# Kernel tuning notes

Hardware: AMD Instinct MI355X
Metric: run time of the kernel (lower is better)

## Reference

```python
import jax, jax.numpy as jnp
import numpy as np

NUM_CAPS_OUT = 10
NUM_NODES = 32 * 6 * 6  # 1152
IN_DIM = 8
OUT_DIM = 16
ROUTING_ITERS = 3


def squash(x):
    # scale = |x|^2/(1+|x|^2); out = scale * x/|x|  (no epsilon, faithful to torch)
    sn = jnp.sum(x * x, axis=-1, keepdims=True)
    return sn / (1.0 + sn) * x / jnp.sqrt(sn)


def setup_inputs() -> dict:
    key = jax.random.key(0)
    ks = jax.random.split(key, 6)
    B = 512
    images = jax.random.normal(ks[0], (B, 1, 28, 28), dtype=jnp.float32)
    # ConvLayer: Conv2d(1, 256, k=9, s=1) with bias
    conv1_w = jax.random.normal(ks[1], (256, 1, 9, 9), dtype=jnp.float32) * 0.05
    conv1_b = jnp.zeros((256,), dtype=jnp.float32)
    prim_w = jax.random.normal(ks[2], (8 * 32, 256, 9, 9), dtype=jnp.float32) * 0.01
    prim_b = jnp.zeros((8 * 32,), dtype=jnp.float32)
    # DigitCaps weight: torch.randn(10, 1152, 8, 16)
    W = jax.random.normal(ks[3], (NUM_CAPS_OUT, NUM_NODES, IN_DIM, OUT_DIM), dtype=jnp.float32)
    return {"images": images, "conv1_w": conv1_w, "conv1_b": conv1_b,
            "prim_w": prim_w, "prim_b": prim_b, "W": W}


def reference(images, conv1_w, conv1_b, prim_w, prim_b, W):
    B = images.shape[0]
    dn = ('NCHW', 'OIHW', 'NCHW')
    # ConvLayer: 28x28 -> 20x20, 256 channels, ReLU
    x = jax.lax.conv_general_dilated(images, conv1_w, (1, 1), 'VALID', dimension_numbers=dn)
    x = jax.nn.relu(x + conv1_b[None, :, None, None])  # [B,256,20,20]
    # PrimaryCaps: 8 stacked convs -> [B, 8*32, 6, 6]; each capsule viewed as (32*6*6,)
    u = jax.lax.conv_general_dilated(x, prim_w, (2, 2), 'VALID', dimension_numbers=dn)
    u = u + prim_b[None, :, None, None]
    u = u.reshape(B, 8, NUM_NODES).transpose(0, 2, 1)  # [B,1152,8]
    u = squash(u)
    # DigitCaps: u_hat[c,b,n,o] = sum_i u[b,n,i] * W[c,n,i,o]
    u_hat = jnp.einsum('bni,cnio->cbno', u, W)  # [10,B,1152,16]
    # Dynamic routing (3 iterations). b_ij kept as [...,1]: torch replicates it
    # across the 16 out dims identically, so math is unchanged.
    b_ij = jnp.zeros(u_hat.shape[:-1] + (1,), dtype=u_hat.dtype)
    v_j = None
    for it in range(ROUTING_ITERS):
        c_ij = jax.nn.softmax(b_ij, axis=2)            # softmax over nodes
        s_j = jnp.sum(c_ij * u_hat, axis=2, keepdims=True)  # [10,B,1,16]
        v_j = squash(s_j)
        if it < ROUTING_ITERS - 1:
            a_ij = jnp.sum(u_hat * v_j, axis=-1, keepdims=True)  # [10,B,1152,1]
            b_ij = b_ij + a_ij
    # squeeze -> [10,B,16], transpose(0,1) -> [B,10,16]
    return v_j[:, :, 0, :].transpose(1, 0, 2)
```

## Files before the change

### kernel.cpp

```cpp
#include <hip/hip_runtime.h>
#include <hip/hip_bf16.h>
#include <cstddef>
#include <cstdint>

typedef __attribute__((ext_vector_type(8))) short v8s;
typedef __attribute__((ext_vector_type(16))) float v16f;

#define GLDS(SRC, DST) __builtin_amdgcn_global_load_lds( \
    (const __attribute__((address_space(1))) void*)(SRC), \
    (__attribute__((address_space(3))) void*)(DST), 16, 0, 0)

#define WAIT_VM6() asm volatile("s_waitcnt vmcnt(6)" ::: "memory")
#define WAIT_VM0() asm volatile("s_waitcnt vmcnt(0)" ::: "memory")
#define SCHED0()   __builtin_amdgcn_sched_barrier(0)

__device__ __forceinline__ void bf16split(float x, unsigned short& h, unsigned short& l) {
    union { float f; unsigned u; } a; a.f = x;
    unsigned r = a.u + 0x7fff + ((a.u >> 16) & 1);
    h = (unsigned short)(r >> 16);
    union { unsigned u; float f; } hb; hb.u = (unsigned)h << 16;
    union { float f; unsigned u; } b; b.f = x - hb.f;
    unsigned r2 = b.u + 0x7fff + ((b.u >> 16) & 1);
    l = (unsigned short)(r2 >> 16);
}

__global__ __launch_bounds__(256) void prep_kernel(
    const float* __restrict__ cw, const float* __restrict__ pw,
    float* __restrict__ wT1, char* __restrict__ wpk)
{
    int idx = blockIdx.x * 256 + threadIdx.x;
    if (idx < 81 * 256) {
        int k = idx >> 8, oc = idx & 255;
        wT1[idx] = cw[oc * 81 + k];
    }
    int Q = idx & 2047;
    int slab = idx >> 11;
    int D = Q << 4;
    int R = D >> 9;
    int off9 = (D & 511) ^ ((R & 31) << 4);
    int h = off9 >> 7, pl = (off9 >> 6) & 1, icb0 = off9 & 63;
    int ch = h * 64 + R;
    int g = slab / 81, k = slab - g * 81;
    int ic0 = g * 32 + (icb0 >> 1);
    const float* src = pw + ((size_t)ch * 256 + ic0) * 81 + k;
    v8s ov;
#pragma unroll
    for (int j = 0; j < 8; ++j) {
        unsigned short hh, ll; bf16split(src[(size_t)j * 81], hh, ll);
        ov[j] = (short)(pl ? ll : hh);
    }
    *(v8s*)(wpk + (size_t)slab * 32768 + D) = ov;
}

__global__ __launch_bounds__(256) void conv1_kernel(
    const float* __restrict__ img,
    const float* __restrict__ wT1,
    const float* __restrict__ bias,
    char* __restrict__ xc2,
    int b0)
{
    const int bl = blockIdx.x;
    const int oc = threadIdx.x;
    __shared__ __align__(16) float im[784];
    const float* ib = img + (size_t)(b0 + bl) * 784;
    for (int e = oc; e < 784; e += 256) im[e] = ib[e];
    float w[81];
#pragma unroll
    for (int k = 0; k < 81; ++k) w[k] = wT1[k * 256 + oc];
    float bv = bias[oc];
    __syncthreads();
    char* ob = xc2 + (size_t)bl * 409600;
    for (int oy = 0; oy < 20; ++oy) {
        float a[20];
#pragma unroll
        for (int ox = 0; ox < 20; ++ox) a[ox] = bv;
        for (int ky = 0; ky < 9; ++ky) {
            const float* rp = &im[(oy + ky) * 28];
            float r[28];
#pragma unroll
            for (int q = 0; q < 7; ++q) {
                float4 v4 = *(const float4*)(rp + q * 4);
                r[q * 4] = v4.x; r[q * 4 + 1] = v4.y;
                r[q * 4 + 2] = v4.z; r[q * 4 + 3] = v4.w;
            }
#pragma unroll
            for (int kx = 0; kx < 9; ++kx) {
                float wv = w[ky * 9 + kx];
#pragma unroll
                for (int ox = 0; ox < 20; ++ox)
                    a[ox] = fmaf(wv, r[ox + kx], a[ox]);
            }
        }
#pragma unroll
        for (int ox = 0; ox < 20; ++ox) {
            float av = fmaxf(a[ox], 0.f);
            unsigned short h, l; bf16split(av, h, l);
            char* rp2 = ob + (size_t)(oy * 20 + ox) * 1024;
            *(unsigned short*)(rp2 + oc * 2) = h;
            *(unsigned short*)(rp2 + 512 + oc * 2) = l;
        }
    }
}

__global__ __launch_bounds__(512, 1) void gemm_kernel(
    const char* __restrict__ xc2,
    const char* __restrict__ wpk,
    float* __restrict__ part,
    int M)
{
    __shared__ __align__(128) char As[3][16384];
    __shared__ __align__(128) char Bs[3][32768];
    const int tid = threadIdx.x;
    const int w = tid >> 6, lane = tid & 63;
    const int wm = w & 1, wn = w >> 1;
    const int col = lane & 31, kg = lane >> 5;
    const int id = blockIdx.x;
    const int g = id & 7;
    const int m0 = (id >> 3) * 128;

    int pbase[2], asrc[2];
#pragma unroll
    for (int i = 0; i < 2; ++i) {
        int d = (w * 2 + i) * 1024 + lane * 16;
        int R = d >> 9;
        int off9 = (d & 511) ^ ((R & 31) << 4);
        int h = off9 >> 7, pl = (off9 >> 6) & 1, w32 = off9 & 63;
        int m = m0 + 32 * h + R;
        if (m >= M) m = M - 1;
        int b = m / 36, s6 = m - b * 36;
        pbase[i] = b * 400 + (s6 / 6) * 40 + (s6 % 6) * 2;
        asrc[i] = pl * 512 + g * 64 + w32;
    }
    const char* wg = wpk + (size_t)g * 81 * 32768;

    v16f acc[2][2];
#pragma unroll
    for (int i = 0; i < 2; ++i)
#pragma unroll
        for (int j = 0; j < 2; ++j)
#pragma unroll
            for (int e = 0; e < 16; ++e) acc[i][j][e] = 0.f;

    auto stage = [&](int nb, int kk) {
        const int koff = (kk / 9) * 20 + (kk % 9);
#pragma unroll
        for (int i = 0; i < 2; ++i)
            GLDS(xc2 + (size_t)(pbase[i] + koff) * 1024 + asrc[i],
                 &As[nb][(w * 2 + i) * 1024]);
        const char* bs = wg + (size_t)kk * 32768;
#pragma unroll
        for (int i = 0; i < 4; ++i)
            GLDS(bs + (w * 4 + i) * 1024 + lane * 16,
                 &Bs[nb][(w * 4 + i) * 1024]);
    };

    stage(0, 0);
    stage(1, 1);
    WAIT_VM6(); SCHED0();
    __builtin_amdgcn_s_barrier(); SCHED0();

    const int xc = col << 4;
    for (int k = 0; k < 81; ++k) {
        const int cur = k % 3;
        if (k + 2 < 81) stage((k + 2) % 3, k + 2);

        const char* Ab = &As[cur][0];
        const char* Bb = &Bs[cur][0];
        v8s Ah[2][2], Al[2][2], Bh[2][2], Bl[2][2];
#pragma unroll
        for (int s = 0; s < 2; ++s) {
            const int vb = s * 32 + kg * 16;
#pragma unroll
            for (int fm = 0; fm < 2; ++fm) {
                const int ho = (wm * 2 + fm) * 128;
                Ah[s][fm] = *(const v8s*)(Ab + col * 512 + ((ho + vb) ^ xc));
                Al[s][fm] = *(const v8s*)(Ab + col * 512 + ((ho + 64 + vb) ^ xc));
            }
#pragma unroll
            for (int fn = 0; fn < 2; ++fn) {
                const char* bp = Bb + (fn * 32 + col) * 512;
                Bh[s][fn] = *(const v8s*)(bp + ((wn * 128 + vb) ^ xc));
                Bl[s][fn] = *(const v8s*)(bp + ((wn * 128 + 64 + vb) ^ xc));
            }
        }
        __builtin_amdgcn_s_setprio(1);
#pragma unroll
        for (int s = 0; s < 2; ++s)
#pragma unroll
            for (int fn = 0; fn < 2; ++fn)
#pragma unroll
                for (int fm = 0; fm < 2; ++fm) {
                    acc[fm][fn] = __builtin_amdgcn_mfma_f32_32x32x16_bf16(Al[s][fm], Bh[s][fn], acc[fm][fn], 0, 0, 0);
                    acc[fm][fn] = __builtin_amdgcn_mfma_f32_32x32x16_bf16(Ah[s][fm], Bl[s][fn], acc[fm][fn], 0, 0, 0);
                    acc[fm][fn] = __builtin_amdgcn_mfma_f32_32x32x16_bf16(Ah[s][fm], Bh[s][fn], acc[fm][fn], 0, 0, 0);
                }
        __builtin_amdgcn_s_setprio(0);

        if (k < 80) {
            if (k < 79) { WAIT_VM6(); } else { WAIT_VM0(); }
            SCHED0();
            __builtin_amdgcn_s_barrier();
            SCHED0();
        }
    }

    float* pg = part + (size_t)g * M * 256;
#pragma unroll
    for (int fm = 0; fm < 2; ++fm)
#pragma unroll
        for (int fn = 0; fn < 2; ++fn) {
            int ch = wn * 64 + fn * 32 + col;
#pragma unroll
            for (int rg = 0; rg < 16; ++rg) {
                int row = (rg & 3) + 8 * (rg >> 2) + 4 * kg;
                int m = m0 + wm * 64 + fm * 32 + row;
                if (m < M) pg[(size_t)m * 256 + ch] = acc[fm][fn][rg];
            }
        }
}

__global__ __launch_bounds__(256) void prim2u_kernel(
    const float* __restrict__ part, const float* __restrict__ pb,
    float* __restrict__ u, int M, int b0)
{
    __shared__ float p[64 * 256];
    __shared__ float bsh[256];
    const int tid = threadIdx.x;
    const int rows0 = blockIdx.x * 64;
    bsh[tid] = pb[tid];
#pragma unroll
    for (int j = 0; j < 16; ++j) {
        int e4 = j * 256 + tid;
        int row = e4 >> 6, c4 = (e4 & 63) << 2;
        int rr = rows0 + row; if (rr >= M) rr = M - 1;
        float4 a = make_float4(0.f, 0.f, 0.f, 0.f);
#pragma unroll
        for (int g = 0; g < 8; ++g) {
            float4 v = *(const float4*)(part + ((size_t)g * M + rr) * 256 + c4);
            a.x += v.x; a.y += v.y; a.z += v.z; a.w += v.w;
        }
        *(float4*)&p[row * 256 + c4] = a;
    }
    __syncthreads();
#pragma unroll
    for (int j = 0; j < 8; ++j) {
        int nt = j * 256 + tid;
        int row = nt >> 5, cc = nt & 31;
        int m = rows0 + row;
        if (m >= M) continue;
        int b = m / 36, s = m - b * 36;
        float p8[8]; float sn = 0.f;
#pragma unroll
        for (int d = 0; d < 8; ++d) {
            float v = p[row * 256 + d * 32 + cc] + bsh[d * 32 + cc];
            p8[d] = v; sn += v * v;
        }
        float fac = sqrtf(sn) / (1.0f + sn);
        float4 o0, o1;
        o0.x = fac * p8[0]; o0.y = fac * p8[1]; o0.z = fac * p8[2]; o0.w = fac * p8[3];
        o1.x = fac * p8[4]; o1.y = fac * p8[5]; o1.z = fac * p8[6]; o1.w = fac * p8[7];
        float* up = u + ((size_t)(b0 + b) * 1152 + cc * 36 + s) * 8;
        *(float4*)up = o0;
        *(float4*)(up + 4) = o1;
    }
}

__global__ __launch_bounds__(512) void routing_kernel(
    const float* __restrict__ u,
    const float* __restrict__ W,
    float* __restrict__ out,
    int B)
{
    const int b0 = blockIdx.x * 2;
    const int c = blockIdx.y;
    const int tid = threadIdx.x;
    __shared__ float uht[2][16][1152];
    __shared__ float bijs[2][1152];
    __shared__ float red[2][4 * 17];
    __shared__ float sred[2][17];
    __shared__ float mred[2][4];

    const float* __restrict__ Wc = W + (size_t)c * (1152 * 128);
    const int b1 = (b0 + 1 < B) ? b0 + 1 : b0;
    const float* __restrict__ ub0 = u + (size_t)b0 * 9216;
    const float* __restrict__ ub1 = u + (size_t)b1 * 9216;

    for (int n = tid; n < 1152; n += 512) {
        const float4* p0 = (const float4*)(ub0 + n * 8);
        const float4* p1 = (const float4*)(ub1 + n * 8);
        float4 a0 = p0[0], a1 = p0[1], c0 = p1[0], c1 = p1[1];
        float uu0[8] = {a0.x, a0.y, a0.z, a0.w, a1.x, a1.y, a1.z, a1.w};
        float uu1[8] = {c0.x, c0.y, c0.z, c0.w, c1.x, c1.y, c1.z, c1.w};
        float acc0[16], acc1[16];
#pragma unroll
        for (int o = 0; o < 16; ++o) { acc0[o] = 0.f; acc1[o] = 0.f; }
        const float* wn = Wc + n * 128;
#pragma unroll
        for (int i = 0; i < 8; ++i)
#pragma unroll
            for (int o = 0; o < 16; ++o) {
                float wv = wn[i * 16 + o];
                acc0[o] = fmaf(uu0[i], wv, acc0[o]);
                acc1[o] = fmaf(uu1[i], wv, acc1[o]);
            }
#pragma unroll
        for (int o = 0; o < 16; ++o) { uht[0][o][n] = acc0[o]; uht[1][o][n] = acc1[o]; }
        bijs[0][n] = 0.f; bijs[1][n] = 0.f;
    }
    __syncthreads();

    const int img = tid >> 8, t = tid & 255;
    const int wid = t >> 6, lane = t & 63;
    const float* __restrict__ UHT = &uht[img][0][0];
    float* __restrict__ bij = bijs[img];
    float* __restrict__ redi = red[img];
    float* __restrict__ sredi = sred[img];
    float* __restrict__ mredi = mred[img];

    float fac = 0.f, inv = 0.f;
    for (int it = 0; it < 3; ++it) {
        float m = -3.4e38f;
        for (int n = t; n < 1152; n += 256) m = fmaxf(m, bij[n]);
#pragma unroll
        for (int off = 32; off > 0; off >>= 1) m = fmaxf(m, __shfl_down(m, off));
        if (lane == 0) mredi[wid] = m;
        __syncthreads();
        float M = fmaxf(fmaxf(mredi[0], mredi[1]), fmaxf(mredi[2], mredi[3]));
        float se = 0.f;
        float sp[16];
#pragma unroll
        for (int o = 0; o < 16; ++o) sp[o] = 0.f;
        for (int n = t; n < 1152; n += 256) {
            float e = expf(bij[n] - M);
            se += e;
#pragma unroll
            for (int o = 0; o < 16; ++o) sp[o] = fmaf(e, UHT[o * 1152 + n], sp[o]);
        }
#pragma unroll
        for (int o = 0; o < 16; ++o)
#pragma unroll
            for (int off = 32; off > 0; off >>= 1) sp[o] += __shfl_down(sp[o], off);
#pragma unroll
        for (int off = 32; off > 0; off >>= 1) se += __shfl_down(se, off);
        if (lane == 0) {
#pragma unroll
            for (int o = 0; o < 16; ++o) redi[wid * 17 + o] = sp[o];
            redi[wid * 17 + 16] = se;
        }
        __syncthreads();
        if (t < 17)
            sredi[t] = redi[t] + redi[17 + t] + redi[34 + t] + redi[51 + t];
        __syncthreads();
        inv = 1.0f / sredi[16];
        float sn = 0.f;
        float sj[16];
#pragma unroll
        for (int o = 0; o < 16; ++o) { sj[o] = sredi[o] * inv; sn = fmaf(sj[o], sj[o], sn); }
        fac = sqrtf(sn) / (1.0f + sn);
        if (it < 2) {
            float v[16];
#pragma unroll
            for (int o = 0; o < 16; ++o) v[o] = fac * sj[o];
            for (int n = t; n < 1152; n += 256) {
                float a = 0.f;
#pragma unroll
                for (int o = 0; o < 16; ++o) a = fmaf(UHT[o * 1152 + n], v[o], a);
                bij[n] += a;
            }
        }
        __syncthreads();
    }
    if (t < 16 && b0 + img < B)
        out[((size_t)(b0 + img) * 10 + c) * 16 + t] = fac * (sredi[t] * inv);
}

extern "C" void kernel_launch(void* const* d_in, const int* in_sizes, int n_in,
                              void* d_out, int out_size, void* d_ws, size_t ws_size,
                              hipStream_t stream) {
    const float* images  = (const float*)d_in[0];
    const float* conv1_w = (const float*)d_in[1];
    const float* conv1_b = (const float*)d_in[2];
    const float* prim_w  = (const float*)d_in[3];
    const float* prim_b  = (const float*)d_in[4];
    const float* W       = (const float*)d_in[5];
    float* out = (float*)d_out;

    const int B = in_sizes[0] / 784;

    char* wsb = (char*)d_ws;
    float* u = (float*)wsb;
    size_t off = (size_t)B * 1152 * 8 * 4;
    float* wT1 = (float*)(wsb + off);
    off += 81 * 256 * 4;
    off = (off + 1023) & ~(size_t)1023;
    char* wpk = wsb + off;
    off += (size_t)648 * 32768;
    size_t rem = (ws_size > off) ? ws_size - off : 0;
    const size_t perimg = 409600 + 294912;
    int Bc = (int)(rem / perimg);
    if (Bc > B) Bc = B;
    if (Bc >= 32) Bc &= ~31;
    if (Bc < 1) Bc = 1;

    prep_kernel<<<5184, 256, 0, stream>>>(conv1_w, prim_w, wT1, wpk);

    for (int b0 = 0; b0 < B; b0 += Bc) {
        int bc = (B - b0 < Bc) ? (B - b0) : Bc;
        char* xc2 = wsb + off;
        float* part = (float*)(xc2 + (size_t)Bc * 409600);
        conv1_kernel<<<bc, 256, 0, stream>>>(images, wT1, conv1_b, xc2, b0);
        int M = bc * 36;
        int Mtiles = (M + 127) / 128;
        gemm_kernel<<<Mtiles * 8, 512, 0, stream>>>(xc2, wpk, part, M);
        prim2u_kernel<<<(M + 63) / 64, 256, 0, stream>>>(part, prim_b, u, M, b0);
    }
    dim3 rg((B + 1) / 2, 10);
    routing_kernel<<<rg, 512, 0, stream>>>(u, W, out, B);
}
```

Baseline: 1.186 ms.

## Enlarge GEMM M-tile to 256 with double buffering and new LDS row swizzle

The primary-caps GEMM block tile grows from 128 to 256 rows. Each wave now computes a 2x4 grid of 32x32 MFMA tiles, which raises reuse of each B fragment loaded from LDS. The 3-stage pipeline with fine-grained vmcnt waits is replaced by a 2-stage double buffer using __syncthreads, and the LDS layout and swizzle for A and B are rearranged to match. prim2u gets a padded LDS row stride and a transposed thread mapping to avoid bank conflicts. The costs are fewer blocks (less parallelism), more accumulator registers, and weaker load/compute overlap.

New measurement: 1.229 ms. 3.6% more time.

```diff
diff --git a/kernel.cpp b/kernel.cpp
--- a/kernel.cpp
+++ b/kernel.cpp
@@ -9,10 +9,6 @@
 #define GLDS(SRC, DST) __builtin_amdgcn_global_load_lds( \
     (const __attribute__((address_space(1))) void*)(SRC), \
     (__attribute__((address_space(3))) void*)(DST), 16, 0, 0)
-
-#define WAIT_VM6() asm volatile("s_waitcnt vmcnt(6)" ::: "memory")
-#define WAIT_VM0() asm volatile("s_waitcnt vmcnt(0)" ::: "memory")
-#define SCHED0()   __builtin_amdgcn_sched_barrier(0)
 
 __device__ __forceinline__ void bf16split(float x, unsigned short& h, unsigned short& l) {
     union { float f; unsigned u; } a; a.f = x;
@@ -37,11 +33,13 @@
     int slab = idx >> 11;
     int D = Q << 4;
     int R = D >> 9;
-    int off9 = (D & 511) ^ ((R & 31) << 4);
-    int h = off9 >> 7, pl = (off9 >> 6) & 1, icb0 = off9 & 63;
-    int ch = h * 64 + R;
+    int v = (D & 511) ^ ((R & 31) << 4);
+    int sub = v >> 7;
+    int ch = R * 4 + sub;
+    int pl = (v >> 6) & 1;
+    int icb = v & 63;
     int g = slab / 81, k = slab - g * 81;
-    int ic0 = g * 32 + (icb0 >> 1);
+    int ic0 = g * 32 + (icb >> 1);
     const float* src = pw + ((size_t)ch * 256 + ic0) * 81 + k;
     v8s ov;
 #pragma unroll
@@ -108,108 +106,104 @@
     float* __restrict__ part,
     int M)
 {
-    __shared__ __align__(128) char As[3][16384];
-    __shared__ __align__(128) char Bs[3][32768];
+    __shared__ __align__(128) char As[2][32768];
+    __shared__ __align__(128) char Bs[2][32768];
     const int tid = threadIdx.x;
     const int w = tid >> 6, lane = tid & 63;
-    const int wm = w & 1, wn = w >> 1;
+    const int wm = w & 3, wn = w >> 2;
     const int col = lane & 31, kg = lane >> 5;
     const int id = blockIdx.x;
     const int g = id & 7;
-    const int m0 = (id >> 3) * 128;
-
-    int pbase[2], asrc[2];
-#pragma unroll
-    for (int i = 0; i < 2; ++i) {
-        int d = (w * 2 + i) * 1024 + lane * 16;
+    const int m0 = (id >> 3) * 256;
+
+    int pbase[4], asrc[4];
+#pragma unroll
+    for (int i = 0; i < 4; ++i) {
+        int d = i * 8192 + w * 1024 + lane * 16;
         int R = d >> 9;
-        int off9 = (d & 511) ^ ((R & 31) << 4);
-        int h = off9 >> 7, pl = (off9 >> 6) & 1, w32 = off9 & 63;
-        int m = m0 + 32 * h + R;
-        if (m >= M) m = M - 1;
+        int v = (d & 511) ^ ((R & 31) << 4);
+        int sub = v >> 7;
+        int mrow = R * 4 + sub;
+        int pl = (v >> 6) & 1;
+        int icb = v & 63;
+        int m = m0 + mrow; if (m >= M) m = M - 1;
         int b = m / 36, s6 = m - b * 36;
         pbase[i] = b * 400 + (s6 / 6) * 40 + (s6 % 6) * 2;
-        asrc[i] = pl * 512 + g * 64 + w32;
+        asrc[i] = pl * 512 + g * 64 + icb;
     }
     const char* wg = wpk + (size_t)g * 81 * 32768;
 
-    v16f acc[2][2];
+    v16f acc[2][4];
 #pragma unroll
     for (int i = 0; i < 2; ++i)
 #pragma unroll
-        for (int j = 0; j < 2; ++j)
+        for (int j = 0; j < 4; ++j)
 #pragma unroll
             for (int e = 0; e < 16; ++e) acc[i][j][e] = 0.f;
 
     auto stage = [&](int nb, int kk) {
         const int koff = (kk / 9) * 20 + (kk % 9);
 #pragma unroll
-        for (int i = 0; i < 2; ++i)
+        for (int i = 0; i < 4; ++i)
             GLDS(xc2 + (size_t)(pbase[i] + koff) * 1024 + asrc[i],
-                 &As[nb][(w * 2 + i) * 1024]);
+                 &As[nb][i * 8192 + w * 1024]);
         const char* bs = wg + (size_t)kk * 32768;
 #pragma unroll
         for (int i = 0; i < 4; ++i)
-            GLDS(bs + (w * 4 + i) * 1024 + lane * 16,
-                 &Bs[nb][(w * 4 + i) * 1024]);
+            GLDS(bs + i * 8192 + w * 1024 + lane * 16,
+                 &Bs[nb][i * 8192 + w * 1024]);
     };
 
     stage(0, 0);
-    stage(1, 1);
-    WAIT_VM6(); SCHED0();
-    __builtin_amdgcn_s_barrier(); SCHED0();
-
-    const int xc = col << 4;
+    __syncthreads();
+
+    const int c2 = col >> 2, sub = col & 3;
+    const int ibA = sub * 128 + kg * 16;
     for (int k = 0; k < 81; ++k) {
-        const int cur = k % 3;
-        if (k + 2 < 81) stage((k + 2) % 3, k + 2);
-
+        const int cur = k & 1;
         const char* Ab = &As[cur][0];
         const char* Bb = &Bs[cur][0];
-        v8s Ah[2][2], Al[2][2], Bh[2][2], Bl[2][2];
+        if (k < 80) stage(cur ^ 1, k + 1);
+
 #pragma unroll
         for (int s = 0; s < 2; ++s) {
-            const int vb = s * 32 + kg * 16;
+            v8s Ah[2], Al[2], Bh[4], Bl[4];
 #pragma unroll
             for (int fm = 0; fm < 2; ++fm) {
-                const int ho = (wm * 2 + fm) * 128;
-                Ah[s][fm] = *(const v8s*)(Ab + col * 512 + ((ho + vb) ^ xc));
-                Al[s][fm] = *(const v8s*)(Ab + col * 512 + ((ho + 64 + vb) ^ xc));
-            }
-#pragma unroll
-            for (int fn = 0; fn < 2; ++fn) {
-                const char* bp = Bb + (fn * 32 + col) * 512;
-                Bh[s][fn] = *(const v8s*)(bp + ((wn * 128 + vb) ^ xc));
-                Bl[s][fn] = *(const v8s*)(bp + ((wn * 128 + 64 + vb) ^ xc));
-            }
-        }
-        __builtin_amdgcn_s_setprio(1);
-#pragma unroll
-        for (int s = 0; s < 2; ++s)
-#pragma unroll
-            for (int fn = 0; fn < 2; ++fn)
+                int R = wm * 16 + fm * 8 + c2;
+                int xr = (R & 31) << 4;
+                const char* ap = Ab + R * 512;
+                Ah[fm] = *(const v8s*)(ap + ((ibA + s * 32) ^ xr));
+                Al[fm] = *(const v8s*)(ap + ((ibA + 64 + s * 32) ^ xr));
+            }
+#pragma unroll
+            for (int fn = 0; fn < 4; ++fn) {
+                int R = wn * 32 + fn * 8 + c2;
+                int xr = (R & 31) << 4;
+                const char* bp = Bb + R * 512;
+                Bh[fn] = *(const v8s*)(bp + ((ibA + s * 32) ^ xr));
+                Bl[fn] = *(const v8s*)(bp + ((ibA + 64 + s * 32) ^ xr));
+            }
+            __builtin_amdgcn_s_setprio(1);
+#pragma unroll
+            for (int fn = 0; fn < 4; ++fn)
 #pragma unroll
                 for (int fm = 0; fm < 2; ++fm) {
-                    acc[fm][fn] = __builtin_amdgcn_mfma_f32_32x32x16_bf16(Al[s][fm], Bh[s][fn], acc[fm][fn], 0, 0, 0);
-                    acc[fm][fn] = __builtin_amdgcn_mfma_f32_32x32x16_bf16(Ah[s][fm], Bl[s][fn], acc[fm][fn], 0, 0, 0);
-                    acc[fm][fn] = __builtin_amdgcn_mfma_f32_32x32x16_bf16(Ah[s][fm], Bh[s][fn], acc[fm][fn], 0, 0, 0);
+                    acc[fm][fn] = __builtin_amdgcn_mfma_f32_32x32x16_bf16(Al[fm], Bh[fn], acc[fm][fn], 0, 0, 0);
+                    acc[fm][fn] = __builtin_amdgcn_mfma_f32_32x32x16_bf16(Ah[fm], Bl[fn], acc[fm][fn], 0, 0, 0);
+                    acc[fm][fn] = __builtin_amdgcn_mfma_f32_32x32x16_bf16(Ah[fm], Bh[fn], acc[fm][fn], 0, 0, 0);
                 }
-        __builtin_amdgcn_s_setprio(0);
-
-        if (k < 80) {
-            if (k < 79) { WAIT_VM6(); } else { WAIT_VM0(); }
-            SCHED0();
-            __builtin_amdgcn_s_barrier();
-            SCHED0();
-        }
+            __builtin_amdgcn_s_setprio(0);
+        }
+        if (k < 80) __syncthreads();
     }
 
     float* pg = part + (size_t)g * M * 256;
 #pragma unroll
     for (int fm = 0; fm < 2; ++fm)
 #pragma unroll
-        for (int fn = 0; fn < 2; ++fn) {
-            int ch = wn * 64 + fn * 32 + col;
+        for (int fn = 0; fn < 4; ++fn) {
+            int ch = wn * 128 + fn * 32 + col;
 #pragma unroll
             for (int rg = 0; rg < 16; ++rg) {
                 int row = (rg & 3) + 8 * (rg >> 2) + 4 * kg;
@@ -223,7 +217,7 @@
     const float* __restrict__ part, const float* __restrict__ pb,
     float* __restrict__ u, int M, int b0)
 {
-    __shared__ float p[64 * 256];
+    __shared__ float p[64 * 257];
     __shared__ float bsh[256];
     const int tid = threadIdx.x;
     const int rows0 = blockIdx.x * 64;
@@ -239,20 +233,21 @@
             float4 v = *(const float4*)(part + ((size_t)g * M + rr) * 256 + c4);
             a.x += v.x; a.y += v.y; a.z += v.z; a.w += v.w;
         }
-        *(float4*)&p[row * 256 + c4] = a;
+        float* pp = &p[row * 257 + c4];
+        pp[0] = a.x; pp[1] = a.y; pp[2] = a.z; pp[3] = a.w;
     }
     __syncthreads();
 #pragma unroll
     for (int j = 0; j < 8; ++j) {
-        int nt = j * 256 + tid;
-        int row = nt >> 5, cc = nt & 31;
+        int idx = j * 256 + tid;
+        int row = idx & 63, cc = idx >> 6;
         int m = rows0 + row;
         if (m >= M) continue;
         int b = m / 36, s = m - b * 36;
         float p8[8]; float sn = 0.f;
 #pragma unroll
         for (int d = 0; d < 8; ++d) {
-            float v = p[row * 256 + d * 32 + cc] + bsh[d * 32 + cc];
+            float v = p[row * 257 + d * 32 + cc] + bsh[d * 32 + cc];
             p8[d] = v; sn += v * v;
         }
         float fac = sqrtf(sn) / (1.0f + sn);
@@ -410,7 +405,7 @@
         float* part = (float*)(xc2 + (size_t)Bc * 409600);
         conv1_kernel<<<bc, 256, 0, stream>>>(images, wT1, conv1_b, xc2, b0);
         int M = bc * 36;
-        int Mtiles = (M + 127) / 128;
+        int Mtiles = (M + 255) / 256;
         gemm_kernel<<<Mtiles * 8, 512, 0, stream>>>(xc2, wpk, part, M);
         prim2u_kernel<<<(M + 63) / 64, 256, 0, stream>>>(part, prim_b, u, M, b0);
     }
```
